# Kernel optimization log

Hardware: AMD Instinct MI355X
Metric: run time of the kernel (lower is better)

## Reference

```python
import jax, jax.numpy as jnp
import numpy as np
from itertools import combinations

ADD = 3  # matches init_kwargs

def setup_inputs() -> dict:
    key = jax.random.key(0)
    x = jax.random.uniform(key, (131072, 16), dtype=jnp.float32)
    return {"x": x}

def reference(x) -> jnp.ndarray:
    n = x.shape[1]
    parts = [x]
    for i in range(2, ADD + 1):
        # static index table of all size-i column subsets: [C(n,i), i]
        idx = jnp.asarray(np.array(list(combinations(range(n), i)), dtype=np.int32))
        # gather + reduce: x[:, idx] -> [N, C, i]; Lukasiewicz t-norm = max(sum - (i-1), 0)
        s = jnp.sum(x[:, idx], axis=2)  # [N, C]
        parts.append(jnp.maximum(s - jnp.float32(i - 1), jnp.float32(0)))
    return jnp.concatenate(parts, axis=1)
```

## Files before the change

kernel.cpp:

```cpp
#include <hip/hip_runtime.h>
#include <hip/hip_bf16.h>


#define NCOLS 696
#define ROWS_PER_BLOCK 256
#define STRIDE_Q 17
#define NCHUNKS 11

typedef float v4f __attribute__((ext_vector_type(4)));

struct Tabs { short a[NCOLS]; short b[NCOLS]; short c[NCOLS]; };

constexpr Tabs make_tabs() {
    Tabs t{};
    int k = 0;
    for (int a = 0; a < 16; ++a) { t.a[k] = (short)a; t.b[k] = -1; t.c[k] = -1; ++k; }
    for (int a = 0; a < 16; ++a)
        for (int b = a + 1; b < 16; ++b) { t.a[k] = (short)a; t.b[k] = (short)b; t.c[k] = -1; ++k; }
    for (int a = 0; a < 16; ++a)
        for (int b = a + 1; b < 16; ++b)
            for (int c = b + 1; c < 16; ++c) { t.a[k] = (short)a; t.b[k] = (short)b; t.c[k] = (short)c; ++k; }
    return t;
}
constexpr Tabs TT = make_tabs();

__device__ __forceinline__ float colval(const float (&xv)[16], int cc) {
    const int a = TT.a[cc], b = TT.b[cc], c = TT.c[cc];
    if (b < 0) return xv[a];
    if (c < 0) return fmaxf(xv[a] + xv[b] - 1.0f, 0.0f);
    return fmaxf(xv[a] + xv[b] + xv[c] - 2.0f, 0.0f);
}

__device__ __forceinline__ void lgkm_fence() {
    __asm__ volatile("s_waitcnt lgkmcnt(0)" ::: "memory");
}

__global__ __launch_bounds__(256, 2)
void luk_kernel(const float* __restrict__ x, float* __restrict__ out) {
    __shared__ v4f lds[ROWS_PER_BLOCK * STRIDE_Q];

    const int t    = threadIdx.x;
    const int wave = t >> 6;
    const int lane = t & 63;
    const size_t row = (size_t)blockIdx.x * ROWS_PER_BLOCK + t;

    float xv[16];
    {
        const v4f* __restrict__ xr = reinterpret_cast<const v4f*>(x + row * 16);
        #pragma unroll
        for (int j = 0; j < 4; ++j) {
            const v4f v = xr[j];
            xv[4 * j + 0] = v.x; xv[4 * j + 1] = v.y;
            xv[4 * j + 2] = v.z; xv[4 * j + 3] = v.w;
        }
    }

    v4f* const myw  = &lds[t * STRIDE_Q];
    const v4f* const rb = &lds[(wave << 6) * STRIDE_Q];
    float* const wbase = out +
        ((size_t)blockIdx.x * ROWS_PER_BLOCK + (size_t)(wave << 6)) * NCOLS;

    #pragma unroll
    for (int ch = 0; ch < NCHUNKS; ++ch) {
        const int Q  = (ch == NCHUNKS - 1) ? 14 : 16;
        const int c0 = ch * 64;

        #pragma unroll
        for (int q = 0; q < Q; ++q) {
            v4f o;
            o.x = colval(xv, c0 + 4 * q + 0);
            o.y = colval(xv, c0 + 4 * q + 1);
            o.z = colval(xv, c0 + 4 * q + 2);
            o.w = colval(xv, c0 + 4 * q + 3);
            myw[q] = o;
        }
        lgkm_fence();

        #pragma unroll
        for (int i = 0; i < 16; ++i) {
            const int r = 4 * i + (lane >> 4);
            const int q = lane & 15;
            if (q < Q) {
                const v4f val = rb[r * STRIDE_Q + q];
                *reinterpret_cast<v4f*>(wbase + (size_t)r * NCOLS + c0 + 4 * q) = val;
            }
        }
        lgkm_fence();
    }
}

extern "C" void kernel_launch(void* const* d_in, const int* in_sizes, int n_in,
                              void* d_out, int out_size, void* d_ws, size_t ws_size,
                              hipStream_t stream) {
    const float* x = (const float*)d_in[0];
    float* out = (float*)d_out;
    const int nrows  = in_sizes[0] / 16;
    const int blocks = nrows / ROWS_PER_BLOCK;
    luk_kernel<<<blocks, 256, 0, stream>>>(x, out);
}
```

Measured before the change: 447.1 us.

## Split output columns of 64 rows across four waves per block

Each block now handles 64 rows instead of 256. Each of its four waves computes a quarter of the 696 output columns for all 64 rows, staging through a small per-wave LDS tile of 4 float4 per lane. This cuts LDS use and raises the occupancy hint to 8 blocks, giving more blocks and shorter per-thread work to hide store latency. The cost is that each wave reloads the same x row per lane, and each transposed store now covers only 4 float4 per row instead of 16, so stores are less contiguous.

```diff
diff --git a/kernel.cpp b/kernel.cpp
--- a/kernel.cpp
+++ b/kernel.cpp
@@ -3,9 +3,6 @@
 
 
 #define NCOLS 696
-#define ROWS_PER_BLOCK 256
-#define STRIDE_Q 17
-#define NCHUNKS 11
 
 typedef float v4f __attribute__((ext_vector_type(4)));
 
@@ -35,18 +32,57 @@
     __asm__ volatile("s_waitcnt lgkmcnt(0)" ::: "memory");
 }
 
-__global__ __launch_bounds__(256, 2)
+template <int W>
+__device__ __forceinline__ void do_quarter(const float (&xv)[16],
+                                           v4f* ldsw,
+                                           float* wbase, int lane) {
+    const int QS = (W == 0) ? 0 : (W == 1) ? 44 : (W == 2) ? 88 : 132;
+    const int QN = (W == 3) ? 42 : 44;
+    const int a  = lane >> 2;
+    const int qq = lane & 3;
+    v4f* const myw = ldsw + lane * 5;
+
+    #pragma unroll
+    for (int ch = 0; ch * 4 < QN; ++ch) {
+        const int q0 = QS + 4 * ch;
+        const int Qc = (QN - 4 * ch >= 4) ? 4 : QN - 4 * ch;
+
+        #pragma unroll
+        for (int q = 0; q < Qc; ++q) {
+            v4f o;
+            o.x = colval(xv, 4 * (q0 + q) + 0);
+            o.y = colval(xv, 4 * (q0 + q) + 1);
+            o.z = colval(xv, 4 * (q0 + q) + 2);
+            o.w = colval(xv, 4 * (q0 + q) + 3);
+            myw[q] = o;
+        }
+        lgkm_fence();
+
+        #pragma unroll
+        for (int i = 0; i < 4; ++i) {
+            const int r = 16 * i + a;
+            if (qq < Qc) {
+                const v4f val = ldsw[r * 5 + qq];
+                *reinterpret_cast<v4f*>(wbase + (size_t)r * NCOLS +
+                                        (size_t)(q0 + qq) * 4) = val;
+            }
+        }
+        lgkm_fence();
+    }
+}
+
+__global__ __launch_bounds__(256, 8)
 void luk_kernel(const float* __restrict__ x, float* __restrict__ out) {
-    __shared__ v4f lds[ROWS_PER_BLOCK * STRIDE_Q];
+    __shared__ v4f lds[4 * 64 * 5];
 
     const int t    = threadIdx.x;
     const int wave = t >> 6;
     const int lane = t & 63;
-    const size_t row = (size_t)blockIdx.x * ROWS_PER_BLOCK + t;
+    const size_t row0 = (size_t)blockIdx.x * 64;
 
     float xv[16];
     {
-        const v4f* __restrict__ xr = reinterpret_cast<const v4f*>(x + row * 16);
+        const v4f* xr = reinterpret_cast<const v4f*>(x + (row0 + (size_t)lane) * 16);
         #pragma unroll
         for (int j = 0; j < 4; ++j) {
             const v4f v = xr[j];
@@ -55,37 +91,14 @@
         }
     }
 
-    v4f* const myw  = &lds[t * STRIDE_Q];
-    const v4f* const rb = &lds[(wave << 6) * STRIDE_Q];
-    float* const wbase = out +
-        ((size_t)blockIdx.x * ROWS_PER_BLOCK + (size_t)(wave << 6)) * NCOLS;
+    v4f* const ldsw = &lds[(size_t)(wave * 64) * 5];
+    float* const wbase = out + row0 * NCOLS;
 
-    #pragma unroll
-    for (int ch = 0; ch < NCHUNKS; ++ch) {
-        const int Q  = (ch == NCHUNKS - 1) ? 14 : 16;
-        const int c0 = ch * 64;
-
-        #pragma unroll
-        for (int q = 0; q < Q; ++q) {
-            v4f o;
-            o.x = colval(xv, c0 + 4 * q + 0);
-            o.y = colval(xv, c0 + 4 * q + 1);
-            o.z = colval(xv, c0 + 4 * q + 2);
-            o.w = colval(xv, c0 + 4 * q + 3);
-            myw[q] = o;
-        }
-        lgkm_fence();
-
-        #pragma unroll
-        for (int i = 0; i < 16; ++i) {
-            const int r = 4 * i + (lane >> 4);
-            const int q = lane & 15;
-            if (q < Q) {
-                const v4f val = rb[r * STRIDE_Q + q];
-                *reinterpret_cast<v4f*>(wbase + (size_t)r * NCOLS + c0 + 4 * q) = val;
-            }
-        }
-        lgkm_fence();
+    switch (wave) {
+        case 0: do_quarter<0>(xv, ldsw, wbase, lane); break;
+        case 1: do_quarter<1>(xv, ldsw, wbase, lane); break;
+        case 2: do_quarter<2>(xv, ldsw, wbase, lane); break;
+        default: do_quarter<3>(xv, ldsw, wbase, lane); break;
     }
 }
 
@@ -95,6 +108,6 @@
     const float* x = (const float*)d_in[0];
     float* out = (float*)d_out;
     const int nrows  = in_sizes[0] / 16;
-    const int blocks = nrows / ROWS_PER_BLOCK;
+    const int blocks = nrows / 64;
     luk_kernel<<<blocks, 256, 0, stream>>>(x, out);
 }
```

Measured after the change: 446.2 us. About the same (-0.2%).
